# Kernel tuning notes

Measured on AMD Instinct MI355X. Metric: run time of the kernel, lower is better.

The kernel has to match this reference:

```python
import jax, jax.numpy as jnp
import numpy as np

N_HEADS = 16

def setup_inputs() -> dict:
    key = jax.random.key(0)
    k1, k2, k3 = jax.random.split(key, 3)
    d = 1024
    x = jax.random.normal(k1, (4, 2048, d), dtype=jnp.float32)
    w_qkv = jax.random.normal(k2, (d, 3 * d), dtype=jnp.float32) * (1.0 / np.sqrt(d))
    w_proj = jax.random.normal(k3, (d, d), dtype=jnp.float32) * (1.0 / np.sqrt(d))
    return {"x": x, "w_qkv": w_qkv, "w_proj": w_proj}

def reference(x, w_qkv, w_proj):
    b, s, c = x.shape
    h = N_HEADS
    hd = c // h
    qkv = x @ w_qkv  # [b, s, 3c]
    q, k, v = jnp.split(qkv, 3, axis=-1)
    # [b, h, s, hd]
    q = q.reshape(b, s, h, hd).transpose(0, 2, 1, 3)
    k = k.reshape(b, s, h, hd).transpose(0, 2, 1, 3)
    v = v.reshape(b, s, h, hd).transpose(0, 2, 1, 3)
    scores = jnp.einsum('bhqd,bhkd->bhqk', q, k) / jnp.sqrt(jnp.float32(hd))
    causal = jnp.tril(jnp.ones((s, s), dtype=bool))
    scores = jnp.where(causal[None, None], scores, jnp.float32(-jnp.inf))
    attn = jax.nn.softmax(scores, axis=-1)
    out = jnp.einsum('bhqk,bhkd->bhqd', attn, v)
    out = out.transpose(0, 2, 1, 3).reshape(b, s, c)
    return out @ w_proj
```

## Files before the change

kernel.cpp:

```cpp
#include <hip/hip_runtime.h>
#include <hip/hip_bf16.h>

typedef unsigned short u16;
typedef __attribute__((ext_vector_type(8))) short short8;
typedef __attribute__((ext_vector_type(4))) float f32x4;
typedef __attribute__((ext_vector_type(16))) float f32x16;

__device__ inline u16 f2bf(float f) {
  unsigned u = __float_as_uint(f);
  u += 0x7fffu + ((u >> 16) & 1u);
  return (u16)(u >> 16);
}

__global__ __launch_bounds__(256) void cast_kernel(const float* __restrict__ in,
                                                   u16* __restrict__ out, int n4) {
  int i = blockIdx.x * 256 + threadIdx.x;
  if (i >= n4) return;
  float4 v = ((const float4*)in)[i];
  ushort4 o;
  o.x = f2bf(v.x); o.y = f2bf(v.y); o.z = f2bf(v.z); o.w = f2bf(v.w);
  ((ushort4*)out)[i] = o;
}

__global__ __launch_bounds__(256) void tcast_kernel(const float* __restrict__ in,
                                                    u16* __restrict__ out, int K, int N) {
  __shared__ float tile[32][33];
  int bx = blockIdx.x * 32;
  int by = blockIdx.y * 32;
  int tx = threadIdx.x & 31, ty = threadIdx.x >> 5;
#pragma unroll
  for (int i = 0; i < 4; i++) {
    int r = ty + i * 8;
    tile[r][tx] = in[(size_t)(by + r) * N + bx + tx];
  }
  __syncthreads();
#pragma unroll
  for (int i = 0; i < 4; i++) {
    int r = ty + i * 8;
    out[(size_t)(bx + r) * K + by + tx] = f2bf(tile[tx][r]);
  }
}


#define VMWAIT(n) asm volatile("s_waitcnt vmcnt(" #n ")" ::: "memory")
#define LGKM0() asm volatile("s_waitcnt lgkmcnt(0)" ::: "memory")
#define BAR() asm volatile("s_barrier" ::: "memory")

__device__ __forceinline__ void gll16(const u16* g, u16* l) {
  __builtin_amdgcn_global_load_lds((const __attribute__((address_space(1))) unsigned*)g,
                                   (__attribute__((address_space(3))) unsigned*)l, 16, 0, 0);
}

__global__ __launch_bounds__(512, 2) void gemm_qkv(const u16* __restrict__ A,
                                                   const u16* __restrict__ Bt,
                                                   u16* __restrict__ qb,
                                                   u16* __restrict__ kpack,
                                                   u16* __restrict__ vpack) {
  __shared__ u16 lds[65536];
  int tid = threadIdx.x;
  int w = tid >> 6, lane = tid & 63, l15 = lane & 15, quad = lane >> 4;
  int wr = w >> 2, wc = w & 3;

  int bid = blockIdx.x;
  int wgid = (bid & 7) * 48 + (bid >> 3);
  int bm = (wgid / 12) * 256;
  int bn3 = (wgid % 12) * 256;

  int srow = lane >> 2;
  int kswz = ((lane & 3) * 8) ^ ((lane >> 5) << 4);
  const u16* gA0 = A + (size_t)(bm + w * 16 + srow) * 1024 + kswz;
  const u16* gA1 = A + (size_t)(bm + 128 + w * 16 + srow) * 1024 + kswz;
  const u16* gB0 = Bt + (size_t)(bn3 + w * 16 + srow) * 1024 + kswz;
  const u16* gB1 = Bt + (size_t)(bn3 + 128 + w * 16 + srow) * 1024 + kswz;

  int kq = (quad * 8) ^ ((l15 & 8) << 1);
  int aoff = wr * 8192 + l15 * 32 + kq;
  int boff = 16384 + (wc >> 1) * 8192 + (wc & 1) * 2048 + l15 * 32 + kq;

  f32x4 acc[8][4];
#pragma unroll
  for (int m = 0; m < 8; m++)
#pragma unroll
    for (int n = 0; n < 4; n++) acc[m][n] = (f32x4)0.0f;

  short8 a[8], bA[4], bB[4];

#define STAGE_AH0(T)                                          \
  do {                                                        \
    u16* d_ = lds + ((T) & 1) * 32768 + w * 512;              \
    gll16(gA0 + (size_t)(T) * 64, d_);                        \
    gll16(gA0 + (size_t)(T) * 64 + 32, d_ + 4096);            \
  } while (0)
#define STAGE_AH1(T)                                          \
  do {                                                        \
    u16* d_ = lds + ((T) & 1) * 32768 + 8192 + w * 512;       \
    gll16(gA1 + (size_t)(T) * 64, d_);                        \
    gll16(gA1 + (size_t)(T) * 64 + 32, d_ + 4096);            \
  } while (0)
#define STAGE_BH0(T)                                          \
  do {                                                        \
    u16* d_ = lds + ((T) & 1) * 32768 + 16384 + w * 512;      \
    gll16(gB0 + (size_t)(T) * 64, d_);                        \
    gll16(gB0 + (size_t)(T) * 64 + 32, d_ + 4096);            \
  } while (0)
#define STAGE_BH1(T)                                          \
  do {                                                        \
    u16* d_ = lds + ((T) & 1) * 32768 + 24576 + w * 512;      \
    gll16(gB1 + (size_t)(T) * 64, d_);                        \
    gll16(gB1 + (size_t)(T) * 64 + 32, d_ + 4096);            \
  } while (0)

#define MFMA16(NLO, BV0, BV1)                                                                  \
  do {                                                                                         \
    __builtin_amdgcn_s_setprio(1);                                                             \
    _Pragma("unroll") for (int m = 0; m < 8; m++)                                              \
        acc[m][NLO] = __builtin_amdgcn_mfma_f32_16x16x32_bf16(a[m], BV0, acc[m][NLO], 0, 0, 0);\
    _Pragma("unroll") for (int m = 0; m < 8; m++)                                              \
        acc[m][NLO + 1] =                                                                      \
            __builtin_amdgcn_mfma_f32_16x16x32_bf16(a[m], BV1, acc[m][NLO + 1], 0, 0, 0);      \
    __builtin_amdgcn_s_setprio(0);                                                             \
  } while (0)

#define PHASE1(T, DOSTG)                                                                       \
  do {                                                                                         \
    const u16* bc_ = lds + ((T) & 1) * 32768;                                                  \
    _Pragma("unroll") for (int m = 0; m < 8; m++)                                              \
        a[m] = *(const short8*)(bc_ + aoff + m * 512);                                         \
    if (DOSTG) STAGE_AH0((T) + 1);                                                             \
    BAR(); LGKM0();                                                                            \
    MFMA16(0, bA[0], bA[1]);                                                                   \
    BAR();                                                                                     \
  } while (0)

#define PHASE2(T, DOSTG)                                                                       \
  do {                                                                                         \
    const u16* bc_ = lds + ((T) & 1) * 32768;                                                  \
    _Pragma("unroll") for (int n = 0; n < 4; n++)                                              \
        bB[n] = *(const short8*)(bc_ + boff + 4096 + n * 512);                                 \
    if (DOSTG) STAGE_AH1((T) + 1);                                                             \
    BAR(); LGKM0();                                                                            \
    MFMA16(2, bA[2], bA[3]);                                                                   \
    BAR();                                                                                     \
  } while (0)

#define PHASE3(T, DOSTG, VMN)                                                                  \
  do {                                                                                         \
    const u16* bc_ = lds + ((T) & 1) * 32768;                                                  \
    _Pragma("unroll") for (int m = 0; m < 8; m++)                                              \
        a[m] = *(const short8*)(bc_ + aoff + 4096 + m * 512);                                  \
    if (DOSTG) STAGE_BH0((T) + 2);                                                             \
    BAR(); LGKM0();                                                                            \
    MFMA16(0, bB[0], bB[1]);                                                                   \
    VMN;                                                                                       \
    BAR();                                                                                     \
  } while (0)

#define PHASE4(T, DORD, DOSTG, VMN)                                                            \
  do {                                                                                         \
    if (DORD) {                                                                                \
      const u16* bn_ = lds + (((T) + 1) & 1) * 32768;                                          \
      _Pragma("unroll") for (int n = 0; n < 4; n++)                                            \
          bA[n] = *(const short8*)(bn_ + boff + n * 512);                                      \
    }                                                                                          \
    if (DOSTG) STAGE_BH1((T) + 2);                                                             \
    BAR(); LGKM0();                                                                            \
    MFMA16(2, bB[2], bB[3]);                                                                   \
    VMN;                                                                                       \
    BAR();                                                                                     \
  } while (0)

  STAGE_BH0(0); STAGE_BH1(0); STAGE_AH0(0); STAGE_AH1(0); STAGE_BH0(1); STAGE_BH1(1);
  VMWAIT(4);
  BAR();
  {
    const u16* bc_ = lds;
#pragma unroll
    for (int n = 0; n < 4; n++) bA[n] = *(const short8*)(bc_ + boff + n * 512);
  }

  for (int T = 0; T < 14; ++T) {
    PHASE1(T, 1);
    PHASE2(T, 1);
    PHASE3(T, 1, VMWAIT(6));
    PHASE4(T, 1, 1, VMWAIT(4));
  }
  PHASE1(14, 1);
  PHASE2(14, 1);
  PHASE3(14, 0, VMWAIT(4));
  PHASE4(14, 1, 0, VMWAIT(0));
  PHASE1(15, 0);
  PHASE2(15, 0);
  PHASE3(15, 0, (void)0);
  PHASE4(15, 0, 0, (void)0);

#undef PHASE1
#undef PHASE2
#undef PHASE3
#undef PHASE4
#undef MFMA16
#undef STAGE_AH0
#undef STAGE_AH1
#undef STAGE_BH0
#undef STAGE_BH1

  if (bn3 < 1024) {
    float scl = 0.18033688011112f;
    int rbase = bm + wr * 128 + quad * 4;
    int cbase = bn3 + wc * 64 + l15;
#pragma unroll
    for (int m = 0; m < 8; m++)
#pragma unroll
      for (int n = 0; n < 4; n++)
#pragma unroll
        for (int r = 0; r < 4; r++)
          qb[(size_t)(rbase + m * 16 + r) * 1024 + cbase + n * 16] = f2bf(acc[m][n][r] * scl);
  } else {
    int bnl = bn3 & 1023;
    int h = (bnl >> 6) + wc;
    int bh = (bm >> 11) * 16 + h;
    int ktb = ((bm & 2047) >> 6) + wr * 2;
    if (bn3 < 2048) {
      int lhi = ((l15 >> 3) & 1) * 32;
      int e = l15 & 7;
#pragma unroll
      for (int m = 0; m < 8; m++) {
        u16* kd = kpack + ((size_t)bh * 32 + ktb + (m >> 2)) * 4096;
        int krb = (m & 3) * 16 + quad * 4;
        int jm = (krb >> 5) * 4;
        int l31b = krb & 31;
#pragma unroll
        for (int n = 0; n < 4; n++)
#pragma unroll
          for (int r = 0; r < 4; r++) {
            int off = (jm + n) * 512 + (l31b + r + lhi) * 8 + e;
            kd[off] = f2bf(acc[m][n][r]);
          }
      }
    } else {
      int e0 = (quad & 1) * 4;
      int hi5 = (quad >> 1) * 32;
#pragma unroll
      for (int m = 0; m < 8; m++) {
        u16* vd = vpack + ((size_t)bh * 32 + ktb + (m >> 2)) * 4096;
#pragma unroll
        for (int n = 0; n < 4; n++) {
          int off = ((n >> 1) * 4 + (m & 3)) * 512 +
                    ((n & 1) * 16 + l15 + hi5) * 8 + e0;
          ushort4 wv;
          wv.x = f2bf(acc[m][n][0]);
          wv.y = f2bf(acc[m][n][1]);
          wv.z = f2bf(acc[m][n][2]);
          wv.w = f2bf(acc[m][n][3]);
          *(ushort4*)(vd + off) = wv;
        }
      }
    }
  }
}

#define GEMM_BODY(KSTR)                                                                       \
  __shared__ __align__(16) u16 As[128 * 32];                                                  \
  __shared__ __align__(16) u16 Bs[128 * 32];                                                  \
  int t = threadIdx.x;                                                                        \
  int wave = t >> 6, lane = t & 63, l15 = lane & 15, quad = lane >> 4;                        \
  int bn = blockIdx.x * 128, bm = blockIdx.y * 128;                                           \
  int wm = (wave >> 1) * 64, wn = (wave & 1) * 64;                                            \
  f32x4 acc[4][4];                                                                            \
  for (int i = 0; i < 4; i++)                                                                 \
    for (int j = 0; j < 4; j++) acc[i][j] = (f32x4)0.0f;                                      \
  int srow = wave * 16 + (lane >> 2);                                                         \
  int scol = (lane & 3) * 8;                                                                  \
  const u16* ga0 = A + (size_t)(bm + srow) * KSTR + scol;                                     \
  const u16* ga1 = A + (size_t)(bm + 64 + srow) * KSTR + scol;                                \
  const u16* gb0 = Bt + (size_t)(bn + srow) * KSTR + scol;                                    \
  const u16* gb1 = Bt + (size_t)(bn + 64 + srow) * KSTR + scol;                               \
  u16* lA0 = As + wave * 512;                                                                 \
  u16* lA1 = As + 2048 + wave * 512;                                                          \
  u16* lB0 = Bs + wave * 512;                                                                 \
  u16* lB1 = Bs + 2048 + wave * 512;                                                          \
  for (int k0 = 0; k0 < KSTR; k0 += 32) {                                                     \
    __syncthreads();                                                                          \
    __builtin_amdgcn_global_load_lds((const __attribute__((address_space(1))) unsigned*)(ga0 + k0), \
                                     (__attribute__((address_space(3))) unsigned*)lA0, 16, 0, 0);   \
    __builtin_amdgcn_global_load_lds((const __attribute__((address_space(1))) unsigned*)(ga1 + k0), \
                                     (__attribute__((address_space(3))) unsigned*)lA1, 16, 0, 0);   \
    __builtin_amdgcn_global_load_lds((const __attribute__((address_space(1))) unsigned*)(gb0 + k0), \
                                     (__attribute__((address_space(3))) unsigned*)lB0, 16, 0, 0);   \
    __builtin_amdgcn_global_load_lds((const __attribute__((address_space(1))) unsigned*)(gb1 + k0), \
                                     (__attribute__((address_space(3))) unsigned*)lB1, 16, 0, 0);   \
    __syncthreads();                                                                          \
    short8 a[4], b[4];                                                                        \
    for (int mt = 0; mt < 4; mt++)                                                            \
      a[mt] = *(const short8*)(&As[(wm + mt * 16 + l15) * 32 + quad * 8]);                    \
    for (int nt = 0; nt < 4; nt++)                                                            \
      b[nt] = *(const short8*)(&Bs[(wn + nt * 16 + l15) * 32 + quad * 8]);                    \
    for (int mt = 0; mt < 4; mt++)                                                            \
      for (int nt = 0; nt < 4; nt++)                                                          \
        acc[mt][nt] = __builtin_amdgcn_mfma_f32_16x16x32_bf16(a[mt], b[nt], acc[mt][nt], 0, 0, 0); \
  }

__global__ __launch_bounds__(256) void gemm_proj(const u16* __restrict__ A,
                                                 const u16* __restrict__ Bt,
                                                 float* __restrict__ Co) {
  GEMM_BODY(1024)
#pragma unroll
  for (int mt = 0; mt < 4; mt++)
#pragma unroll
    for (int nt = 0; nt < 4; nt++)
#pragma unroll
      for (int r = 0; r < 4; r++) {
        int row = bm + wm + mt * 16 + quad * 4 + r;
        int col = bn + wn + nt * 16 + l15;
        Co[(size_t)row * 1024 + col] = acc[mt][nt][r];
      }
}

__global__ __launch_bounds__(256, 2) void attn_kernel(const u16* __restrict__ qbuf,
                                                      const u16* __restrict__ kpack,
                                                      const u16* __restrict__ vpack,
                                                      u16* __restrict__ ctx) {
  int t = threadIdx.x;
  int wave = t >> 6, lane = t & 63, l31 = lane & 31, hi = lane >> 5;
  int bh = blockIdx.x;
  int s = (int)blockIdx.y * 4 + wave;
  int b = bh >> 4, h = bh & 15;
  int rowbase = b * 2048;
  int hi4 = hi * 4;

  const u16* kp = kpack + (size_t)bh * (32 * 4096) + lane * 8;
  const u16* vp = vpack + (size_t)bh * (32 * 4096) + lane * 8;

#pragma unroll
  for (int ph = 0; ph < 2; ph++) {
    int strip = ph ? 63 - s : s;
    int q0 = strip * 32;
    int q_lane = q0 + l31;

    const u16* qp = qbuf + (size_t)(rowbase + q_lane) * 1024 + h * 64 + hi * 8;
    short8 qf[4];
#pragma unroll
    for (int ks = 0; ks < 4; ks++) qf[ks] = *(const short8*)(qp + ks * 16);

    float l_run = 0.0f;
    f32x16 o[2];
    o[0] = (f32x16)0.0f; o[1] = (f32x16)0.0f;
    int ktmax = (q0 + 31) >> 6;

    for (int kt = 0; kt <= ktmax; kt++) {
      const u16* kb = kp + kt * 4096;
      const u16* vb = vp + kt * 4096;

      short8 ka[8], vv[8];
#pragma unroll
      for (int j = 0; j < 8; j++) {
        ka[j] = *(const short8*)(kb + j * 512);
        vv[j] = *(const short8*)(vb + j * 512);
      }

      f32x16 st0 = (f32x16)0.0f, st1 = (f32x16)0.0f;
#pragma unroll
      for (int ks = 0; ks < 4; ks++) {
        st0 = __builtin_amdgcn_mfma_f32_32x32x16_bf16(ka[ks], qf[ks], st0, 0, 0, 0);
        st1 = __builtin_amdgcn_mfma_f32_32x32x16_bf16(ka[4 + ks], qf[ks], st1, 0, 0, 0);
      }

      unsigned pk[2][8];
      if (kt == ktmax) {
#pragma unroll
        for (int ii = 0; ii < 8; ii++) {
          int key = kt * 64 + ((2 * ii) & 3) + 8 * ((2 * ii) >> 2) + hi4;
          float p00 = (key     <= q_lane) ? __builtin_amdgcn_exp2f(st0[2 * ii])     : 0.0f;
          float p01 = (key + 1 <= q_lane) ? __builtin_amdgcn_exp2f(st0[2 * ii + 1]) : 0.0f;
          float p10 = (key + 32 <= q_lane) ? __builtin_amdgcn_exp2f(st1[2 * ii])     : 0.0f;
          float p11 = (key + 33 <= q_lane) ? __builtin_amdgcn_exp2f(st1[2 * ii + 1]) : 0.0f;
          l_run += p00 + p01 + p10 + p11;
          pk[0][ii] = ((__float_as_uint(p00) + 0x8000u) >> 16) |
                      ((__float_as_uint(p01) + 0x8000u) & 0xffff0000u);
          pk[1][ii] = ((__float_as_uint(p10) + 0x8000u) >> 16) |
                      ((__float_as_uint(p11) + 0x8000u) & 0xffff0000u);
        }
      } else {
#pragma unroll
        for (int ii = 0; ii < 8; ii++) {
          float p00 = __builtin_amdgcn_exp2f(st0[2 * ii]);
          float p01 = __builtin_amdgcn_exp2f(st0[2 * ii + 1]);
          float p10 = __builtin_amdgcn_exp2f(st1[2 * ii]);
          float p11 = __builtin_amdgcn_exp2f(st1[2 * ii + 1]);
          l_run += p00 + p01 + p10 + p11;
          pk[0][ii] = ((__float_as_uint(p00) + 0x8000u) >> 16) |
                      ((__float_as_uint(p01) + 0x8000u) & 0xffff0000u);
          pk[1][ii] = ((__float_as_uint(p10) + 0x8000u) >> 16) |
                      ((__float_as_uint(p11) + 0x8000u) & 0xffff0000u);
        }
      }

      short8 pf[4];
#pragma unroll
      for (int ks2 = 0; ks2 < 4; ks2++) {
        int km = ks2 >> 1, h4 = (ks2 & 1) * 4;
        unsigned A0 = pk[km][h4 + 0], A1 = pk[km][h4 + 1];
        unsigned B0 = pk[km][h4 + 2], B1 = pk[km][h4 + 3];
        unsigned tA0 = (unsigned)__shfl_xor((int)A0, 32);
        unsigned tA1 = (unsigned)__shfl_xor((int)A1, 32);
        unsigned tB0 = (unsigned)__shfl_xor((int)B0, 32);
        unsigned tB1 = (unsigned)__shfl_xor((int)B1, 32);
        union { unsigned u[4]; short8 sh; } fr;
        fr.u[0] = hi ? tB0 : A0;
        fr.u[1] = hi ? tB1 : A1;
        fr.u[2] = hi ? B0 : tA0;
        fr.u[3] = hi ? B1 : tA1;
        pf[ks2] = fr.sh;
      }

#pragma unroll
      for (int am = 0; am < 2; am++)
#pragma unroll
        for (int ks2 = 0; ks2 < 4; ks2++)
          o[am] = __builtin_amdgcn_mfma_f32_32x32x16_bf16(vv[am * 4 + ks2], pf[ks2], o[am], 0, 0, 0);
    }

    float l_tot = l_run + __shfl_xor(l_run, 32);
    float inv = 1.0f / l_tot;
    size_t obase = (size_t)(rowbase + q_lane) * 1024 + h * 64;
#pragma unroll
    for (int am = 0; am < 2; am++)
#pragma unroll
      for (int k = 0; k < 4; k++) {
        ushort4 w;
        w.x = f2bf(o[am][4 * k + 0] * inv);
        w.y = f2bf(o[am][4 * k + 1] * inv);
        w.z = f2bf(o[am][4 * k + 2] * inv);
        w.w = f2bf(o[am][4 * k + 3] * inv);
        *(ushort4*)&ctx[obase + am * 32 + k * 8 + hi4] = w;
      }
  }
}

extern "C" void kernel_launch(void* const* d_in, const int* in_sizes, int n_in,
                              void* d_out, int out_size, void* d_ws, size_t ws_size,
                              hipStream_t stream) {
  const float* x      = (const float*)d_in[0];
  const float* w_qkv  = (const float*)d_in[1];
  const float* w_proj = (const float*)d_in[2];
  float* out = (float*)d_out;

  char* ws = (char*)d_ws;
  const size_t MB = 1024 * 1024;
  u16* qbuf   = (u16*)(ws);
  u16* kpack  = (u16*)(ws + 16 * MB);
  u16* vpack  = (u16*)(ws + 32 * MB);
  u16* xb     = (u16*)(ws + 48 * MB);
  u16* ctx    = (u16*)(ws + 64 * MB);
  u16* wqkvT  = (u16*)(ws + 80 * MB);
  u16* wprojT = (u16*)(ws + 86 * MB);

  cast_kernel<<<8192, 256, 0, stream>>>(x, xb, 2097152);
  tcast_kernel<<<dim3(96, 32), 256, 0, stream>>>(w_qkv, wqkvT, 1024, 3072);
  tcast_kernel<<<dim3(32, 32), 256, 0, stream>>>(w_proj, wprojT, 1024, 1024);

  gemm_qkv<<<dim3(384), 512, 0, stream>>>(xb, wqkvT, qbuf, kpack, vpack);
  attn_kernel<<<dim3(64, 8), 256, 0, stream>>>(qbuf, kpack, vpack, ctx);
  gemm_proj<<<dim3(8, 64), 256, 0, stream>>>(ctx, wprojT, out);
}
```

Baseline: 242.8 us.

## Pipeline output projection GEMM and merge cast kernels into one launch

```diff
diff --git a/kernel.cpp b/kernel.cpp
--- a/kernel.cpp
+++ b/kernel.cpp
@@ -12,21 +12,32 @@
   return (u16)(u >> 16);
 }
 
-__global__ __launch_bounds__(256) void cast_kernel(const float* __restrict__ in,
-                                                   u16* __restrict__ out, int n4) {
-  int i = blockIdx.x * 256 + threadIdx.x;
-  if (i >= n4) return;
-  float4 v = ((const float4*)in)[i];
-  ushort4 o;
-  o.x = f2bf(v.x); o.y = f2bf(v.y); o.z = f2bf(v.z); o.w = f2bf(v.w);
-  ((ushort4*)out)[i] = o;
-}
-
-__global__ __launch_bounds__(256) void tcast_kernel(const float* __restrict__ in,
-                                                    u16* __restrict__ out, int K, int N) {
+__global__ __launch_bounds__(256) void prep_kernel(const float* __restrict__ x,
+                                                   u16* __restrict__ xb,
+                                                   const float* __restrict__ wq,
+                                                   u16* __restrict__ wqT,
+                                                   const float* __restrict__ wp,
+                                                   u16* __restrict__ wpT) {
   __shared__ float tile[32][33];
-  int bx = blockIdx.x * 32;
-  int by = blockIdx.y * 32;
+  int bid = blockIdx.x;
+  if (bid < 8192) {
+    int i = bid * 256 + threadIdx.x;
+    float4 v = ((const float4*)x)[i];
+    ushort4 o;
+    o.x = f2bf(v.x); o.y = f2bf(v.y); o.z = f2bf(v.z); o.w = f2bf(v.w);
+    ((ushort4*)xb)[i] = o;
+    return;
+  }
+  const float* in; u16* out; int N, bx, by;
+  if (bid < 11264) {
+    int idx = bid - 8192;
+    in = wq; out = wqT; N = 3072;
+    bx = (idx % 96) * 32; by = (idx / 96) * 32;
+  } else {
+    int idx = bid - 11264;
+    in = wp; out = wpT; N = 1024;
+    bx = (idx % 32) * 32; by = (idx / 32) * 32;
+  }
   int tx = threadIdx.x & 31, ty = threadIdx.x >> 5;
 #pragma unroll
   for (int i = 0; i < 4; i++) {
@@ -37,10 +48,9 @@
 #pragma unroll
   for (int i = 0; i < 4; i++) {
     int r = ty + i * 8;
-    out[(size_t)(bx + r) * K + by + tx] = f2bf(tile[tx][r]);
-  }
-}
-
+    out[(size_t)(bx + r) * 1024 + by + tx] = f2bf(tile[tx][r]);
+  }
+}
 
 #define VMWAIT(n) asm volatile("s_waitcnt vmcnt(" #n ")" ::: "memory")
 #define LGKM0() asm volatile("s_waitcnt lgkmcnt(0)" ::: "memory")
@@ -258,61 +268,156 @@
   }
 }
 
-#define GEMM_BODY(KSTR)                                                                       \
-  __shared__ __align__(16) u16 As[128 * 32];                                                  \
-  __shared__ __align__(16) u16 Bs[128 * 32];                                                  \
-  int t = threadIdx.x;                                                                        \
-  int wave = t >> 6, lane = t & 63, l15 = lane & 15, quad = lane >> 4;                        \
-  int bn = blockIdx.x * 128, bm = blockIdx.y * 128;                                           \
-  int wm = (wave >> 1) * 64, wn = (wave & 1) * 64;                                            \
-  f32x4 acc[4][4];                                                                            \
-  for (int i = 0; i < 4; i++)                                                                 \
-    for (int j = 0; j < 4; j++) acc[i][j] = (f32x4)0.0f;                                      \
-  int srow = wave * 16 + (lane >> 2);                                                         \
-  int scol = (lane & 3) * 8;                                                                  \
-  const u16* ga0 = A + (size_t)(bm + srow) * KSTR + scol;                                     \
-  const u16* ga1 = A + (size_t)(bm + 64 + srow) * KSTR + scol;                                \
-  const u16* gb0 = Bt + (size_t)(bn + srow) * KSTR + scol;                                    \
-  const u16* gb1 = Bt + (size_t)(bn + 64 + srow) * KSTR + scol;                               \
-  u16* lA0 = As + wave * 512;                                                                 \
-  u16* lA1 = As + 2048 + wave * 512;                                                          \
-  u16* lB0 = Bs + wave * 512;                                                                 \
-  u16* lB1 = Bs + 2048 + wave * 512;                                                          \
-  for (int k0 = 0; k0 < KSTR; k0 += 32) {                                                     \
-    __syncthreads();                                                                          \
-    __builtin_amdgcn_global_load_lds((const __attribute__((address_space(1))) unsigned*)(ga0 + k0), \
-                                     (__attribute__((address_space(3))) unsigned*)lA0, 16, 0, 0);   \
-    __builtin_amdgcn_global_load_lds((const __attribute__((address_space(1))) unsigned*)(ga1 + k0), \
-                                     (__attribute__((address_space(3))) unsigned*)lA1, 16, 0, 0);   \
-    __builtin_amdgcn_global_load_lds((const __attribute__((address_space(1))) unsigned*)(gb0 + k0), \
-                                     (__attribute__((address_space(3))) unsigned*)lB0, 16, 0, 0);   \
-    __builtin_amdgcn_global_load_lds((const __attribute__((address_space(1))) unsigned*)(gb1 + k0), \
-                                     (__attribute__((address_space(3))) unsigned*)lB1, 16, 0, 0);   \
-    __syncthreads();                                                                          \
-    short8 a[4], b[4];                                                                        \
-    for (int mt = 0; mt < 4; mt++)                                                            \
-      a[mt] = *(const short8*)(&As[(wm + mt * 16 + l15) * 32 + quad * 8]);                    \
-    for (int nt = 0; nt < 4; nt++)                                                            \
-      b[nt] = *(const short8*)(&Bs[(wn + nt * 16 + l15) * 32 + quad * 8]);                    \
-    for (int mt = 0; mt < 4; mt++)                                                            \
-      for (int nt = 0; nt < 4; nt++)                                                          \
-        acc[mt][nt] = __builtin_amdgcn_mfma_f32_16x16x32_bf16(a[mt], b[nt], acc[mt][nt], 0, 0, 0); \
-  }
-
-__global__ __launch_bounds__(256) void gemm_proj(const u16* __restrict__ A,
-                                                 const u16* __restrict__ Bt,
-                                                 float* __restrict__ Co) {
-  GEMM_BODY(1024)
-#pragma unroll
-  for (int mt = 0; mt < 4; mt++)
-#pragma unroll
-    for (int nt = 0; nt < 4; nt++)
-#pragma unroll
-      for (int r = 0; r < 4; r++) {
-        int row = bm + wm + mt * 16 + quad * 4 + r;
-        int col = bn + wn + nt * 16 + l15;
-        Co[(size_t)row * 1024 + col] = acc[mt][nt][r];
-      }
+__global__ __launch_bounds__(512, 2) void gemm_proj(const u16* __restrict__ A,
+                                                    const u16* __restrict__ Bt,
+                                                    float* __restrict__ Co) {
+  __shared__ u16 lds[49152];
+  int tid = threadIdx.x;
+  int w = tid >> 6, lane = tid & 63, l15 = lane & 15, quad = lane >> 4;
+  int wr = w >> 1, wc = w & 1;
+
+  int bid = blockIdx.x;
+  int wgid = (bid & 7) * 32 + (bid >> 3);
+  int bm = (wgid >> 3) * 256;
+  int bn = (wgid & 7) * 128;
+
+  int srow = lane >> 2;
+  int kswz = ((lane & 3) * 8) ^ ((lane >> 5) << 4);
+  const u16* gA0 = A + (size_t)(bm + w * 16 + srow) * 1024 + kswz;
+  const u16* gA1 = A + (size_t)(bm + 128 + w * 16 + srow) * 1024 + kswz;
+  const u16* gB0 = Bt + (size_t)(bn + w * 16 + srow) * 1024 + kswz;
+
+  int kq = (quad * 8) ^ ((l15 & 8) << 1);
+  int aoff = (wr >> 1) * 8192 + (wr & 1) * 2048 + l15 * 32 + kq;
+  int boff = 16384 + wc * 2048 + l15 * 32 + kq;
+
+  f32x4 acc[4][4];
+#pragma unroll
+  for (int m = 0; m < 4; m++)
+#pragma unroll
+    for (int n = 0; n < 4; n++) acc[m][n] = (f32x4)0.0f;
+
+  short8 a[4], bA[4], bB[4];
+
+#define PSTG_ALO(T)                                           \
+  do {                                                        \
+    u16* d_ = lds + ((T) & 1) * 24576 + w * 512;              \
+    gll16(gA0 + (size_t)(T) * 64, d_);                        \
+    gll16(gA0 + (size_t)(T) * 64 + 32, d_ + 4096);            \
+  } while (0)
+#define PSTG_AHI(T)                                           \
+  do {                                                        \
+    u16* d_ = lds + ((T) & 1) * 24576 + 8192 + w * 512;       \
+    gll16(gA1 + (size_t)(T) * 64, d_);                        \
+    gll16(gA1 + (size_t)(T) * 64 + 32, d_ + 4096);            \
+  } while (0)
+#define PSTG_B(T)                                             \
+  do {                                                        \
+    u16* d_ = lds + ((T) & 1) * 24576 + 16384 + w * 512;      \
+    gll16(gB0 + (size_t)(T) * 64, d_);                        \
+    gll16(gB0 + (size_t)(T) * 64 + 32, d_ + 4096);            \
+  } while (0)
+
+#define MFMA8(NLO, BV0, BV1)                                                                   \
+  do {                                                                                         \
+    __builtin_amdgcn_s_setprio(1);                                                             \
+    _Pragma("unroll") for (int m = 0; m < 4; m++)                                              \
+        acc[m][NLO] = __builtin_amdgcn_mfma_f32_16x16x32_bf16(a[m], BV0, acc[m][NLO], 0, 0, 0);\
+    _Pragma("unroll") for (int m = 0; m < 4; m++)                                              \
+        acc[m][NLO + 1] =                                                                      \
+            __builtin_amdgcn_mfma_f32_16x16x32_bf16(a[m], BV1, acc[m][NLO + 1], 0, 0, 0);      \
+    __builtin_amdgcn_s_setprio(0);                                                             \
+  } while (0)
+
+#define PPH1(T, DOSTG)                                                                         \
+  do {                                                                                         \
+    const u16* bc_ = lds + ((T) & 1) * 24576;                                                  \
+    _Pragma("unroll") for (int m = 0; m < 4; m++)                                              \
+        a[m] = *(const short8*)(bc_ + aoff + m * 512);                                         \
+    if (DOSTG) PSTG_ALO((T) + 1);                                                              \
+    BAR(); LGKM0();                                                                            \
+    MFMA8(0, bA[0], bA[1]);                                                                    \
+    BAR();                                                                                     \
+  } while (0)
+
+#define PPH2(T, DOSTG)                                                                         \
+  do {                                                                                         \
+    const u16* bc_ = lds + ((T) & 1) * 24576;                                                  \
+    _Pragma("unroll") for (int n = 0; n < 4; n++)                                              \
+        bB[n] = *(const short8*)(bc_ + boff + 4096 + n * 512);                                 \
+    if (DOSTG) PSTG_AHI((T) + 1);                                                              \
+    BAR(); LGKM0();                                                                            \
+    MFMA8(2, bA[2], bA[3]);                                                                    \
+    BAR();                                                                                     \
+  } while (0)
+
+#define PPH3(T, DOSTG, VMN)                                                                    \
+  do {                                                                                         \
+    const u16* bc_ = lds + ((T) & 1) * 24576;                                                  \
+    _Pragma("unroll") for (int m = 0; m < 4; m++)                                              \
+        a[m] = *(const short8*)(bc_ + aoff + 4096 + m * 512);                                  \
+    if (DOSTG) PSTG_B((T) + 2);                                                                \
+    BAR(); LGKM0();                                                                            \
+    MFMA8(0, bB[0], bB[1]);                                                                    \
+    VMN;                                                                                       \
+    BAR();                                                                                     \
+  } while (0)
+
+#define PPH4(T, DORD, VMN)                                                                     \
+  do {                                                                                         \
+    if (DORD) {                                                                                \
+      const u16* bn_ = lds + (((T) + 1) & 1) * 24576;                                          \
+      _Pragma("unroll") for (int n = 0; n < 4; n++)                                            \
+          bA[n] = *(const short8*)(bn_ + boff + n * 512);                                      \
+    }                                                                                          \
+    BAR(); LGKM0();                                                                            \
+    MFMA8(2, bB[2], bB[3]);                                                                    \
+    VMN;                                                                                       \
+    BAR();                                                                                     \
+  } while (0)
+
+  PSTG_ALO(0); PSTG_AHI(0); PSTG_B(0); PSTG_B(1);
+  VMWAIT(2);
+  BAR();
+  {
+    const u16* bc_ = lds;
+#pragma unroll
+    for (int n = 0; n < 4; n++) bA[n] = *(const short8*)(bc_ + boff + n * 512);
+  }
+
+  for (int T = 0; T < 14; ++T) {
+    PPH1(T, 1);
+    PPH2(T, 1);
+    PPH3(T, 1, VMWAIT(6));
+    PPH4(T, 1, VMWAIT(2));
+  }
+  PPH1(14, 1);
+  PPH2(14, 1);
+  PPH3(14, 0, VMWAIT(4));
+  PPH4(14, 1, VMWAIT(0));
+  PPH1(15, 0);
+  PPH2(15, 0);
+  PPH3(15, 0, (void)0);
+  PPH4(15, 0, (void)0);
+
+#undef PPH1
+#undef PPH2
+#undef PPH3
+#undef PPH4
+#undef MFMA8
+#undef PSTG_ALO
+#undef PSTG_AHI
+#undef PSTG_B
+
+  int rbase = bm + wr * 64 + quad * 4;
+  int cbase = bn + wc * 64 + l15;
+#pragma unroll
+  for (int m = 0; m < 4; m++)
+#pragma unroll
+    for (int n = 0; n < 4; n++)
+#pragma unroll
+      for (int r = 0; r < 4; r++)
+        Co[(size_t)(rbase + m * 16 + r) * 1024 + cbase + n * 16] = acc[m][n][r];
 }
 
 __global__ __launch_bounds__(256, 2) void attn_kernel(const u16* __restrict__ qbuf,
@@ -454,11 +559,8 @@
   u16* wqkvT  = (u16*)(ws + 80 * MB);
   u16* wprojT = (u16*)(ws + 86 * MB);
 
-  cast_kernel<<<8192, 256, 0, stream>>>(x, xb, 2097152);
-  tcast_kernel<<<dim3(96, 32), 256, 0, stream>>>(w_qkv, wqkvT, 1024, 3072);
-  tcast_kernel<<<dim3(32, 32), 256, 0, stream>>>(w_proj, wprojT, 1024, 1024);
-
+  prep_kernel<<<12288, 256, 0, stream>>>(x, xb, w_qkv, wqkvT, w_proj, wprojT);
   gemm_qkv<<<dim3(384), 512, 0, stream>>>(xb, wqkvT, qbuf, kpack, vpack);
   attn_kernel<<<dim3(64, 8), 256, 0, stream>>>(qbuf, kpack, vpack, ctx);
-  gemm_proj<<<dim3(8, 64), 256, 0, stream>>>(ctx, wprojT, out);
-}
+  gemm_proj<<<dim3(256), 512, 0, stream>>>(ctx, wprojT, out);
+}
```

Result: faster. 234.5 us (-3.4%).
